# Performance work log

Measured on AMD Instinct MI355X. Metric: run time of the kernel, lower is better.

## Reference

```python
import jax, jax.numpy as jnp
import numpy as np

N = 131072   # total nodes
E = 262144   # directed edges (avg degree 2, molecular graphs)
G = 4096     # number of graphs in the batch
H = 64       # hidden_dim


def _linear_init(key, fan_in, fan_out):
    # torch.nn.Linear default: U(-1/sqrt(fan_in), 1/sqrt(fan_in))
    s = 1.0 / np.sqrt(fan_in)
    kw, kb = jax.random.split(key)
    W = jax.random.uniform(kw, (fan_in, fan_out), jnp.float32, -s, s)
    b = jax.random.uniform(kb, (fan_out,), jnp.float32, -s, s)
    return W, b


def setup_inputs() -> dict:
    key = jax.random.key(0)
    ks = jax.random.split(key, 8)
    d = {}
    d["x"] = jax.random.normal(ks[0], (N, 1), jnp.float32)
    d["edge_index"] = jax.random.randint(ks[1], (2, E), 0, N, jnp.int32)
    d["batch"] = jnp.sort(jax.random.randint(ks[2], (N,), 0, G, jnp.int32))
    d["W1"], d["b1"] = _linear_init(ks[3], 1, H)          # GCNConv(1, 64)
    d["W2"], d["b2"] = _linear_init(ks[4], H, 2 * H)       # GCNConv(64, 128)
    d["W3"], d["b3"] = _linear_init(ks[5], 2 * H, 4 * H)   # GCNConv(128, 256)
    d["fc1_W"], d["fc1_b"] = _linear_init(ks[6], 4 * H, 128)
    d["fc2_W"], d["fc2_b"] = _linear_init(ks[7], 128, 12)
    return d


def gcn_conv(x, W, b, src, dst):
    """PyG GCNConv: D^-1/2 (A + I) D^-1/2 (x W) + b, self-loops added."""
    h = x @ W                                                   # [N, out]
    deg = jax.ops.segment_sum(jnp.ones(E, jnp.float32), dst, num_segments=N) + 1.0
    dinv = jax.lax.rsqrt(deg)                                   # [N]
    coef = dinv[src] * dinv[dst]                                # [E]
    agg = jax.ops.segment_sum(h[src] * coef[:, None], dst, num_segments=N)
    agg = agg + h * (dinv * dinv)[:, None]                      # self-loop term: h_i / deg_i
    return agg + b


def reference(x, edge_index, batch, W1, b1, W2, b2, W3, b3, fc1_W, fc1_b, fc2_W, fc2_b):
    src, dst = edge_index[0], edge_index[1]
    h = jax.nn.relu(gcn_conv(x, W1, b1, src, dst))
    h = jax.nn.relu(gcn_conv(h, W2, b2, src, dst))
    h = gcn_conv(h, W3, b3, src, dst)                            # [N, 256]
    # global_mean_pool over batch ids
    sums = jax.ops.segment_sum(h, batch, num_segments=G)         # [G, 256]
    cnts = jax.ops.segment_sum(jnp.ones(N, jnp.float32), batch, num_segments=G)
    g = sums / jnp.maximum(cnts, 1.0)[:, None]
    g = jax.nn.relu(g @ fc1_W + fc1_b)
    return g @ fc2_W + fc2_b                                     # [G, 12]
```

## Files before the change

### kernel.cpp

```cpp
#include <hip/hip_runtime.h>
#include <hip/hip_fp16.h>

#define NN 131072
#define EE 262144
#define GG 4096

typedef _Float16 h2v __attribute__((ext_vector_type(2)));

#if __has_builtin(__builtin_amdgcn_fdot2)
#define FDOT2(a, b, c) __builtin_amdgcn_fdot2((a), (b), (c), false)
#else
#define FDOT2(a, b, c) ((float)(a)[0] * (float)(b)[0] + (float)(a)[1] * (float)(b)[1] + (c))
#endif

__global__ void k_zero(int4* __restrict__ p, int n4) {
    int i = blockIdx.x * 256 + threadIdx.x;
    if (i < n4) p[i] = make_int4(0, 0, 0, 0);
}

__global__ void k_count(const int* __restrict__ dst, int* __restrict__ indeg) {
    int e = blockIdx.x * 256 + threadIdx.x;
    if (e < EE) atomicAdd(&indeg[dst[e]], 1);
}

__global__ __launch_bounds__(256) void k_scan_a(const int* __restrict__ indeg,
                                                int* __restrict__ bsum,
                                                float* __restrict__ dinv,
                                                const int* __restrict__ batch,
                                                int* __restrict__ gstart) {
    __shared__ int red[256];
    int tid = threadIdx.x;
    int gid = blockIdx.x * 256 + tid;
    int v = indeg[gid];
    dinv[gid] = rsqrtf((float)v + 1.0f);
    red[tid] = v;
    {
        int b1v = batch[gid];
        int b0v = (gid == 0) ? -1 : batch[gid - 1];
        for (int g = b0v + 1; g <= b1v; ++g) gstart[g] = gid;
        if (gid == NN - 1)
            for (int g = b1v + 1; g <= GG; ++g) gstart[g] = NN;
    }
    __syncthreads();
#pragma unroll
    for (int off = 128; off > 0; off >>= 1) {
        if (tid < off) red[tid] += red[tid + off];
        __syncthreads();
    }
    if (tid == 0) bsum[blockIdx.x] = red[0];
}

__global__ __launch_bounds__(512) void k_scan_b(const int* __restrict__ bsum,
                                                int* __restrict__ boff) {
    __shared__ int ps[512];
    int tid = threadIdx.x;
    ps[tid] = bsum[tid];
    __syncthreads();
    for (int off = 1; off < 512; off <<= 1) {
        int v = (tid >= off) ? ps[tid - off] : 0;
        __syncthreads();
        ps[tid] += v;
        __syncthreads();
    }
    boff[tid] = (tid > 0) ? ps[tid - 1] : 0;
    if (tid == 511) boff[512] = ps[511];
}

__global__ __launch_bounds__(256) void k_scan_c(const int* __restrict__ indeg,
                                                const int* __restrict__ boff,
                                                int* __restrict__ rowptr,
                                                int* __restrict__ cursor) {
    __shared__ int ps[256];
    int tid = threadIdx.x;
    int gid = blockIdx.x * 256 + tid;
    int v = indeg[gid];
    ps[tid] = v;
    __syncthreads();
    for (int off = 1; off < 256; off <<= 1) {
        int t = (tid >= off) ? ps[tid - off] : 0;
        __syncthreads();
        ps[tid] += t;
        __syncthreads();
    }
    int excl = boff[blockIdx.x] + ps[tid] - v;
    rowptr[gid] = excl;
    cursor[gid] = excl;
    if (gid == NN - 1) rowptr[NN] = boff[512];
}

__global__ void k_fill_edges(const int* __restrict__ src, const int* __restrict__ dst,
                             const float* __restrict__ dinv,
                             int* __restrict__ cursor, int* __restrict__ ecol,
                             float* __restrict__ ecoef) {
    int e = blockIdx.x * 256 + threadIdx.x;
    if (e < EE) {
        int d = dst[e], s = src[e];
        int slot = atomicAdd(&cursor[d], 1);
        ecol[slot] = s;
        ecoef[slot] = dinv[d] * dinv[s];
    }
}

__global__ void k_z(const float* __restrict__ x, const float* __restrict__ dinv,
                    const int* __restrict__ rowptr, const int* __restrict__ ecol,
                    const float* __restrict__ ecoef, float* __restrict__ z) {
    int i = blockIdx.x * 256 + threadIdx.x;
    if (i < NN) {
        float di = dinv[i];
        float s = x[i] * di * di;
        int e0 = rowptr[i], e1 = rowptr[i + 1];
        for (int e = e0; e < e1; ++e) s += ecoef[e] * x[ecol[e]];
        z[i] = s;
    }
}

__global__ __launch_bounds__(256) void k_gemm2u(const float* __restrict__ z,
                                                const float* __restrict__ dinv,
                                                const int* __restrict__ rowptr,
                                                const int* __restrict__ ecol,
                                                const float* __restrict__ ecoef,
                                                const float* __restrict__ W1,
                                                const float* __restrict__ b1,
                                                const float* __restrict__ W2,
                                                const float* __restrict__ b2,
                                                __half* __restrict__ rh) {
    __shared__ h2v At[64][33];
    __shared__ h2v Wt[32][128];
    __shared__ float w1s[64], b1s[64];

    int tid = threadIdx.x;
    int i0 = blockIdx.x * 64;

    if (tid < 64) { w1s[tid] = W1[tid]; b1s[tid] = b1[tid]; }
    {
        int c4 = tid & 31, kp0 = tid >> 5;
#pragma unroll
        for (int p = 0; p < 4; ++p) {
            int kp = kp0 + p * 8;
            const float4 lo = *(const float4*)&W2[(size_t)(2 * kp) * 128 + c4 * 4];
            const float4 hi = *(const float4*)&W2[(size_t)(2 * kp + 1) * 128 + c4 * 4];
            h2v h0, h1, h2_, h3;
            h0[0] = (_Float16)lo.x; h0[1] = (_Float16)hi.x;
            h1[0] = (_Float16)lo.y; h1[1] = (_Float16)hi.y;
            h2_[0] = (_Float16)lo.z; h2_[1] = (_Float16)hi.z;
            h3[0] = (_Float16)lo.w; h3[1] = (_Float16)hi.w;
            Wt[kp][c4 * 4 + 0] = h0;
            Wt[kp][c4 * 4 + 1] = h1;
            Wt[kp][c4 * 4 + 2] = h2_;
            Wt[kp][c4 * 4 + 3] = h3;
        }
    }
    __syncthreads();

    {
        int n = tid >> 2;
        int kp0 = (tid & 3) * 8;
        int i = i0 + n;
        float zi = z[i], di = dinv[i];
        float d2 = di * di;
        float uacc[16];
#pragma unroll
        for (int j = 0; j < 16; ++j)
            uacc[j] = d2 * fmaxf(zi * w1s[kp0 * 2 + j] + b1s[kp0 * 2 + j], 0.f);
        int e0 = rowptr[i], e1 = rowptr[i + 1];
        for (int e = e0; e < e1; ++e) {
            float w = ecoef[e];
            float zs = z[ecol[e]];
#pragma unroll
            for (int j = 0; j < 16; ++j)
                uacc[j] += w * fmaxf(zs * w1s[kp0 * 2 + j] + b1s[kp0 * 2 + j], 0.f);
        }
#pragma unroll
        for (int j2 = 0; j2 < 8; ++j2) {
            h2v h;
            h[0] = (_Float16)uacc[2 * j2];
            h[1] = (_Float16)uacc[2 * j2 + 1];
            At[n][kp0 + j2] = h;
        }
    }
    __syncthreads();

    int colg = tid & 15;
    int rowg = tid >> 4;
    float acc[4][8];
#pragma unroll
    for (int rr = 0; rr < 4; ++rr)
#pragma unroll
        for (int c = 0; c < 8; ++c) acc[rr][c] = 0.0f;

#pragma unroll 4
    for (int kp = 0; kp < 32; ++kp) {
        h2v a2[4];
#pragma unroll
        for (int rr = 0; rr < 4; ++rr) a2[rr] = At[rowg * 4 + rr][kp];
        h2v wv[8];
        *(float4*)&wv[0] = *(const float4*)&Wt[kp][colg * 4];
        *(float4*)&wv[4] = *(const float4*)&Wt[kp][64 + colg * 4];
#pragma unroll
        for (int rr = 0; rr < 4; ++rr)
#pragma unroll
            for (int c = 0; c < 8; ++c)
                acc[rr][c] = FDOT2(a2[rr], wv[c], acc[rr][c]);
    }

#pragma unroll
    for (int rr = 0; rr < 4; ++rr) {
        int i = i0 + rowg * 4 + rr;
#pragma unroll
        for (int h = 0; h < 2; ++h) {
            int j = h * 64 + colg * 4;
            const float4 b = *(const float4*)&b2[j];
            __half2 p0 = __floats2half2_rn(fmaxf(acc[rr][h * 4 + 0] + b.x, 0.f),
                                           fmaxf(acc[rr][h * 4 + 1] + b.y, 0.f));
            __half2 p1 = __floats2half2_rn(fmaxf(acc[rr][h * 4 + 2] + b.z, 0.f),
                                           fmaxf(acc[rr][h * 4 + 3] + b.w, 0.f));
            union { __half2 h2[2]; float2 f; } u;
            u.h2[0] = p0; u.h2[1] = p1;
            *(float2*)&rh[(size_t)i * 128 + j] = u.f;
        }
    }
}

__device__ inline void ldr8(const __half* __restrict__ rh, size_t idx, float* o) {
    union { float4 f; __half2 h[4]; } u;
    u.f = *(const float4*)&rh[idx];
#pragma unroll
    for (int q = 0; q < 4; ++q) {
        float2 t = __half22float2(u.h[q]);
        o[q * 2] = t.x; o[q * 2 + 1] = t.y;
    }
}

__global__ __launch_bounds__(256) void k_pool(const __half* __restrict__ rh,
                                              const float* __restrict__ dinv,
                                              const int* __restrict__ rowptr,
                                              const int* __restrict__ ecol,
                                              const float* __restrict__ ecoef,
                                              const int* __restrict__ gstart,
                                              float* __restrict__ Y,
                                              float* __restrict__ cntf) {
    int g = blockIdx.x, tid = threadIdx.x;
    int lo = gstart[g], hi = gstart[g + 1];
    int cnt = hi - lo;

    int lane = tid & 15, ty = tid >> 4;
    int c = lane * 8;
    float acc[8];
#pragma unroll
    for (int q = 0; q < 8; ++q) acc[q] = 0.f;
    float v0[8], v1[8], v2[8], v3[8];

    int i = lo + ty;
    for (; i + 16 < hi; i += 32) {
        float d0 = dinv[i], d1 = dinv[i + 16];
        ldr8(rh, (size_t)i * 128 + c, v0);
        ldr8(rh, (size_t)(i + 16) * 128 + c, v1);
        float w0 = d0 * d0, w1 = d1 * d1;
#pragma unroll
        for (int q = 0; q < 8; ++q) acc[q] += v0[q] * w0 + v1[q] * w1;
    }
    for (; i < hi; i += 16) {
        float di = dinv[i], d2 = di * di;
        ldr8(rh, (size_t)i * 128 + c, v0);
#pragma unroll
        for (int q = 0; q < 8; ++q) acc[q] += v0[q] * d2;
    }

    int e0 = rowptr[lo], e1 = rowptr[hi];
    int e = e0 + ty;
    for (; e + 48 < e1; e += 64) {
        int s0 = ecol[e], s1 = ecol[e + 16], s2 = ecol[e + 32], s3 = ecol[e + 48];
        float w0 = ecoef[e], w1 = ecoef[e + 16], w2 = ecoef[e + 32], w3 = ecoef[e + 48];
        ldr8(rh, (size_t)s0 * 128 + c, v0);
        ldr8(rh, (size_t)s1 * 128 + c, v1);
        ldr8(rh, (size_t)s2 * 128 + c, v2);
        ldr8(rh, (size_t)s3 * 128 + c, v3);
#pragma unroll
        for (int q = 0; q < 8; ++q)
            acc[q] += v0[q] * w0 + v1[q] * w1 + v2[q] * w2 + v3[q] * w3;
    }
    for (; e < e1; e += 16) {
        int s = ecol[e];
        float w = ecoef[e];
        ldr8(rh, (size_t)s * 128 + c, v0);
#pragma unroll
        for (int q = 0; q < 8; ++q) acc[q] += v0[q] * w;
    }

    __shared__ float red[16][128];
    *(float4*)&red[ty][c]     = make_float4(acc[0], acc[1], acc[2], acc[3]);
    *(float4*)&red[ty][c + 4] = make_float4(acc[4], acc[5], acc[6], acc[7]);
    __syncthreads();
    if (tid < 128) {
        float s = 0.0f;
#pragma unroll
        for (int t = 0; t < 16; ++t) s += red[t][tid];
        float inv = (cnt > 0) ? 1.0f / (float)cnt : 0.0f;
        Y[(size_t)g * 128 + tid] = s * inv;
    }
    if (tid == 0) cntf[g] = (float)cnt;
}

template <int K, int OUTW, bool RELU_OUT, bool GUARD>
__global__ __launch_bounds__(256) void k_gemm(const float* __restrict__ A,
                                              const float* __restrict__ W,
                                              const float* __restrict__ bias,
                                              const float* __restrict__ cntf,
                                              float* __restrict__ C) {
    __shared__ float At[64][68];
    __shared__ float Wt[64][128];

    int tid  = threadIdx.x;
    int colg = tid & 15;
    int rowg = tid >> 4;
    int i0 = blockIdx.x * 64;
    int j0 = blockIdx.y * 128;

    float acc[4][8];
#pragma unroll
    for (int r = 0; r < 4; ++r)
#pragma unroll
        for (int c = 0; c < 8; ++c) acc[r][c] = 0.0f;

    for (int k0 = 0; k0 < K; k0 += 64) {
        __syncthreads();
        {
            int k4 = tid & 15, r0 = tid >> 4;
#pragma unroll
            for (int p = 0; p < 4; ++p) {
                int r = r0 + p * 16;
                *(float4*)&At[r][k4 * 4] =
                    *(const float4*)&A[(size_t)(i0 + r) * K + k0 + k4 * 4];
            }
        }
        {
            int c4 = tid & 31, kk0 = tid >> 5;
#pragma unroll
            for (int p = 0; p < 8; ++p) {
                int kk = kk0 + p * 8;
                *(float4*)&Wt[kk][c4 * 4] =
                    *(const float4*)&W[(size_t)(k0 + kk) * OUTW + j0 + c4 * 4];
            }
        }
        __syncthreads();
#pragma unroll 4
        for (int kk = 0; kk < 64; ++kk) {
            float a[4];
#pragma unroll
            for (int r = 0; r < 4; ++r) a[r] = At[rowg * 4 + r][kk];
            const float4 w0 = *(const float4*)&Wt[kk][colg * 4];
            const float4 w1 = *(const float4*)&Wt[kk][64 + colg * 4];
            float w[8] = {w0.x, w0.y, w0.z, w0.w, w1.x, w1.y, w1.z, w1.w};
#pragma unroll
            for (int r = 0; r < 4; ++r)
#pragma unroll
                for (int c = 0; c < 8; ++c) acc[r][c] += a[r] * w[c];
        }
    }

#pragma unroll
    for (int r = 0; r < 4; ++r) {
        int i = i0 + rowg * 4 + r;
        float flag = 1.0f;
        if (GUARD) flag = (cntf[i] > 0.0f) ? 1.0f : 0.0f;
#pragma unroll
        for (int h = 0; h < 2; ++h) {
            int j = j0 + h * 64 + colg * 4;
            const float4 b = *(const float4*)&bias[j];
            float4 v;
            v.x = acc[r][h * 4 + 0] + b.x * flag;
            v.y = acc[r][h * 4 + 1] + b.y * flag;
            v.z = acc[r][h * 4 + 2] + b.z * flag;
            v.w = acc[r][h * 4 + 3] + b.w * flag;
            if (RELU_OUT) {
                v.x = fmaxf(v.x, 0.f); v.y = fmaxf(v.y, 0.f);
                v.z = fmaxf(v.z, 0.f); v.w = fmaxf(v.w, 0.f);
            }
            *(float4*)&C[(size_t)i * OUTW + j] = v;
        }
    }
}

__global__ __launch_bounds__(256) void k_fc12(const float* __restrict__ A,
                                              const float* __restrict__ W,
                                              const float* __restrict__ bias,
                                              const float* __restrict__ fc2W,
                                              const float* __restrict__ fc2b,
                                              float* __restrict__ out) {
    __shared__ float At[64][68];
    __shared__ float Wt[64][128];

    int tid  = threadIdx.x;
    int colg = tid & 15;
    int rowg = tid >> 4;
    int i0 = blockIdx.x * 64;

    float acc[4][8];
#pragma unroll
    for (int r = 0; r < 4; ++r)
#pragma unroll
        for (int c = 0; c < 8; ++c) acc[r][c] = 0.0f;

    for (int k0 = 0; k0 < 256; k0 += 64) {
        __syncthreads();
        {
            int k4 = tid & 15, r0 = tid >> 4;
#pragma unroll
            for (int p = 0; p < 4; ++p) {
                int r = r0 + p * 16;
                *(float4*)&At[r][k4 * 4] =
                    *(const float4*)&A[(size_t)(i0 + r) * 256 + k0 + k4 * 4];
            }
        }
        {
            int c4 = tid & 31, kk0 = tid >> 5;
#pragma unroll
            for (int p = 0; p < 8; ++p) {
                int kk = kk0 + p * 8;
                *(float4*)&Wt[kk][c4 * 4] =
                    *(const float4*)&W[(size_t)(k0 + kk) * 128 + c4 * 4];
            }
        }
        __syncthreads();
#pragma unroll 4
        for (int kk = 0; kk < 64; ++kk) {
            float a[4];
#pragma unroll
            for (int r = 0; r < 4; ++r) a[r] = At[rowg * 4 + r][kk];
            const float4 w0 = *(const float4*)&Wt[kk][colg * 4];
            const float4 w1 = *(const float4*)&Wt[kk][64 + colg * 4];
            float w[8] = {w0.x, w0.y, w0.z, w0.w, w1.x, w1.y, w1.z, w1.w};
#pragma unroll
            for (int r = 0; r < 4; ++r)
#pragma unroll
                for (int c = 0; c < 8; ++c) acc[r][c] += a[r] * w[c];
        }
    }
    __syncthreads();
    float* g1s = &Wt[0][0];
    float* w2s = &At[0][0];
    for (int idx = tid; idx < 128 * 12; idx += 256) w2s[idx] = fc2W[idx];

#pragma unroll
    for (int r = 0; r < 4; ++r) {
        int row = rowg * 4 + r;
#pragma unroll
        for (int h = 0; h < 2; ++h) {
            int j = h * 64 + colg * 4;
            const float4 b = *(const float4*)&bias[j];
            float4 v;
            v.x = fmaxf(acc[r][h * 4 + 0] + b.x, 0.f);
            v.y = fmaxf(acc[r][h * 4 + 1] + b.y, 0.f);
            v.z = fmaxf(acc[r][h * 4 + 2] + b.z, 0.f);
            v.w = fmaxf(acc[r][h * 4 + 3] + b.w, 0.f);
            *(float4*)&g1s[row * 128 + j] = v;
        }
    }
    __syncthreads();
    for (int idx = tid; idx < 64 * 12; idx += 256) {
        int row = idx / 12, col = idx % 12;
        float o = fc2b[col];
        const float* gr = &g1s[row * 128];
        for (int k = 0; k < 128; ++k) o += gr[k] * w2s[k * 12 + col];
        out[(size_t)(i0 + row) * 12 + col] = o;
    }
}

extern "C" void kernel_launch(void* const* d_in, const int* in_sizes, int n_in,
                              void* d_out, int out_size, void* d_ws, size_t ws_size,
                              hipStream_t stream) {
    const float* x     = (const float*)d_in[0];
    const int*   ei    = (const int*)d_in[1];
    const int*   batch = (const int*)d_in[2];
    const float* W1    = (const float*)d_in[3];
    const float* b1    = (const float*)d_in[4];
    const float* W2    = (const float*)d_in[5];
    const float* b2    = (const float*)d_in[6];
    const float* W3    = (const float*)d_in[7];
    const float* b3    = (const float*)d_in[8];
    const float* fc1W  = (const float*)d_in[9];
    const float* fc1b  = (const float*)d_in[10];
    const float* fc2W  = (const float*)d_in[11];
    const float* fc2b  = (const float*)d_in[12];
    float* out = (float*)d_out;

    const int* srcp = ei;
    const int* dstp = ei + EE;

    float* ws     = (float*)d_ws;
    __half* rh    = (__half*)ws;
    float* Y      = ws + (size_t)NN * 64;
    float* pooled = Y + (size_t)GG * 128;
    float* cntf   = pooled + (size_t)GG * 256;
    float* dinv   = cntf + GG;
    float* zbuf   = dinv + NN;
    float* ecoef  = zbuf + NN;
    int* indeg  = (int*)(ecoef + EE);
    int* rowptr = indeg + NN;
    int* cursor = rowptr + NN + 4;
    int* ecol   = cursor + NN;
    int* bsum   = ecol + EE;
    int* boff   = bsum + 512;
    int* gstart = boff + 516;

    k_zero<<<NN / 4 / 256, 256, 0, stream>>>((int4*)indeg, NN / 4);
    k_count<<<EE / 256, 256, 0, stream>>>(dstp, indeg);
    k_scan_a<<<NN / 256, 256, 0, stream>>>(indeg, bsum, dinv, batch, gstart);
    k_scan_b<<<1, 512, 0, stream>>>(bsum, boff);
    k_scan_c<<<NN / 256, 256, 0, stream>>>(indeg, boff, rowptr, cursor);
    k_fill_edges<<<EE / 256, 256, 0, stream>>>(srcp, dstp, dinv, cursor, ecol, ecoef);

    k_z<<<NN / 256, 256, 0, stream>>>(x, dinv, rowptr, ecol, ecoef, zbuf);

    k_gemm2u<<<NN / 64, 256, 0, stream>>>(zbuf, dinv, rowptr, ecol, ecoef,
                                          W1, b1, W2, b2, rh);

    k_pool<<<GG, 256, 0, stream>>>(rh, dinv, rowptr, ecol, ecoef, gstart, Y, cntf);

    k_gemm<128, 256, false, true><<<dim3(GG / 64, 2), 256, 0, stream>>>(
        Y, W3, b3, cntf, pooled);
    k_fc12<<<GG / 64, 256, 0, stream>>>(pooled, fc1W, fc1b, fc2W, fc2b, out);
}
```

Baseline: 130.4 us.

## Fuse CSR build and first aggregation into one cooperative kernel with grid syncs

Replaces seven small kernel launches (zeroing, degree counting, three scan phases, edge fill, first-layer aggregation) with a single cooperative kernel of 512 blocks that separates the phases with grid-wide barriers. The aim is to remove per-launch overhead and inter-kernel gaps in the front-end. In exchange it depends on all 512 blocks being co-resident, and grid.sync may cost as much as the launches it replaces.

```diff
diff --git a/kernel.cpp b/kernel.cpp
--- a/kernel.cpp
+++ b/kernel.cpp
@@ -1,5 +1,8 @@
 #include <hip/hip_runtime.h>
 #include <hip/hip_fp16.h>
+#include <hip/hip_cooperative_groups.h>
+
+namespace cg = cooperative_groups;
 
 #define NN 131072
 #define EE 262144
@@ -13,99 +16,106 @@
 #define FDOT2(a, b, c) ((float)(a)[0] * (float)(b)[0] + (float)(a)[1] * (float)(b)[1] + (c))
 #endif
 
-__global__ void k_zero(int4* __restrict__ p, int n4) {
-    int i = blockIdx.x * 256 + threadIdx.x;
-    if (i < n4) p[i] = make_int4(0, 0, 0, 0);
-}
-
-__global__ void k_count(const int* __restrict__ dst, int* __restrict__ indeg) {
-    int e = blockIdx.x * 256 + threadIdx.x;
-    if (e < EE) atomicAdd(&indeg[dst[e]], 1);
-}
-
-__global__ __launch_bounds__(256) void k_scan_a(const int* __restrict__ indeg,
-                                                int* __restrict__ bsum,
-                                                float* __restrict__ dinv,
-                                                const int* __restrict__ batch,
-                                                int* __restrict__ gstart) {
-    __shared__ int red[256];
-    int tid = threadIdx.x;
-    int gid = blockIdx.x * 256 + tid;
-    int v = indeg[gid];
-    dinv[gid] = rsqrtf((float)v + 1.0f);
-    red[tid] = v;
-    {
+__global__ __launch_bounds__(256) void k_front(const int* __restrict__ src,
+                                               const int* __restrict__ dst,
+                                               const float* __restrict__ x,
+                                               const int* __restrict__ batch,
+                                               int* __restrict__ indeg,
+                                               int* __restrict__ bsum,
+                                               int* __restrict__ boff,
+                                               float* __restrict__ dinv,
+                                               int* __restrict__ gstart,
+                                               int* __restrict__ rowptr,
+                                               int* __restrict__ cursor,
+                                               int* __restrict__ ecol,
+                                               float* __restrict__ ecoef,
+                                               float* __restrict__ z) {
+    cg::grid_group grid = cg::this_grid();
+    int tid = threadIdx.x, b = blockIdx.x;
+    __shared__ int sh[256];
+
+    indeg[b * 256 + tid] = 0;
+    grid.sync();
+
+    {
+        int e = b * 512 + tid;
+        atomicAdd(&indeg[dst[e]], 1);
+        atomicAdd(&indeg[dst[e + 256]], 1);
+    }
+    grid.sync();
+
+    {
+        int gid = b * 256 + tid;
+        int v = indeg[gid];
+        dinv[gid] = rsqrtf((float)v + 1.0f);
         int b1v = batch[gid];
         int b0v = (gid == 0) ? -1 : batch[gid - 1];
         for (int g = b0v + 1; g <= b1v; ++g) gstart[g] = gid;
         if (gid == NN - 1)
             for (int g = b1v + 1; g <= GG; ++g) gstart[g] = NN;
-    }
-    __syncthreads();
-#pragma unroll
-    for (int off = 128; off > 0; off >>= 1) {
-        if (tid < off) red[tid] += red[tid + off];
-        __syncthreads();
-    }
-    if (tid == 0) bsum[blockIdx.x] = red[0];
-}
-
-__global__ __launch_bounds__(512) void k_scan_b(const int* __restrict__ bsum,
-                                                int* __restrict__ boff) {
-    __shared__ int ps[512];
-    int tid = threadIdx.x;
-    ps[tid] = bsum[tid];
-    __syncthreads();
-    for (int off = 1; off < 512; off <<= 1) {
-        int v = (tid >= off) ? ps[tid - off] : 0;
-        __syncthreads();
-        ps[tid] += v;
-        __syncthreads();
-    }
-    boff[tid] = (tid > 0) ? ps[tid - 1] : 0;
-    if (tid == 511) boff[512] = ps[511];
-}
-
-__global__ __launch_bounds__(256) void k_scan_c(const int* __restrict__ indeg,
-                                                const int* __restrict__ boff,
-                                                int* __restrict__ rowptr,
-                                                int* __restrict__ cursor) {
-    __shared__ int ps[256];
-    int tid = threadIdx.x;
-    int gid = blockIdx.x * 256 + tid;
-    int v = indeg[gid];
-    ps[tid] = v;
-    __syncthreads();
-    for (int off = 1; off < 256; off <<= 1) {
-        int t = (tid >= off) ? ps[tid - off] : 0;
-        __syncthreads();
-        ps[tid] += t;
-        __syncthreads();
-    }
-    int excl = boff[blockIdx.x] + ps[tid] - v;
-    rowptr[gid] = excl;
-    cursor[gid] = excl;
-    if (gid == NN - 1) rowptr[NN] = boff[512];
-}
-
-__global__ void k_fill_edges(const int* __restrict__ src, const int* __restrict__ dst,
-                             const float* __restrict__ dinv,
-                             int* __restrict__ cursor, int* __restrict__ ecol,
-                             float* __restrict__ ecoef) {
-    int e = blockIdx.x * 256 + threadIdx.x;
-    if (e < EE) {
-        int d = dst[e], s = src[e];
-        int slot = atomicAdd(&cursor[d], 1);
-        ecol[slot] = s;
-        ecoef[slot] = dinv[d] * dinv[s];
-    }
-}
-
-__global__ void k_z(const float* __restrict__ x, const float* __restrict__ dinv,
-                    const int* __restrict__ rowptr, const int* __restrict__ ecol,
-                    const float* __restrict__ ecoef, float* __restrict__ z) {
-    int i = blockIdx.x * 256 + threadIdx.x;
-    if (i < NN) {
+        sh[tid] = v;
+        __syncthreads();
+#pragma unroll
+        for (int off = 128; off > 0; off >>= 1) {
+            if (tid < off) sh[tid] += sh[tid + off];
+            __syncthreads();
+        }
+        if (tid == 0) bsum[b] = sh[0];
+        __syncthreads();
+    }
+    grid.sync();
+
+    if (b == 0) {
+        int a0 = bsum[2 * tid], a1 = bsum[2 * tid + 1];
+        int pair = a0 + a1;
+        sh[tid] = pair;
+        __syncthreads();
+        for (int off = 1; off < 256; off <<= 1) {
+            int v = (tid >= off) ? sh[tid - off] : 0;
+            __syncthreads();
+            sh[tid] += v;
+            __syncthreads();
+        }
+        int incl = sh[tid];
+        int excl = incl - pair;
+        boff[2 * tid] = excl;
+        boff[2 * tid + 1] = excl + a0;
+        if (tid == 255) boff[512] = incl;
+    }
+    grid.sync();
+
+    {
+        int gid = b * 256 + tid;
+        int v = indeg[gid];
+        sh[tid] = v;
+        __syncthreads();
+        for (int off = 1; off < 256; off <<= 1) {
+            int t2 = (tid >= off) ? sh[tid - off] : 0;
+            __syncthreads();
+            sh[tid] += t2;
+            __syncthreads();
+        }
+        int excl = boff[b] + sh[tid] - v;
+        rowptr[gid] = excl;
+        cursor[gid] = excl;
+        if (gid == NN - 1) rowptr[NN] = boff[512];
+    }
+    grid.sync();
+
+    {
+#pragma unroll
+        for (int q = 0; q < 2; ++q) {
+            int e = b * 512 + tid + q * 256;
+            int d = dst[e], s = src[e];
+            int slot = atomicAdd(&cursor[d], 1);
+            ecol[slot] = s;
+            ecoef[slot] = dinv[d] * dinv[s];
+        }
+    }
+    grid.sync();
+
+    {
+        int i = b * 256 + tid;
         float di = dinv[i];
         float s = x[i] * di * di;
         int e0 = rowptr[i], e1 = rowptr[i + 1];
@@ -503,14 +513,16 @@
     int* boff   = bsum + 512;
     int* gstart = boff + 516;
 
-    k_zero<<<NN / 4 / 256, 256, 0, stream>>>((int4*)indeg, NN / 4);
-    k_count<<<EE / 256, 256, 0, stream>>>(dstp, indeg);
-    k_scan_a<<<NN / 256, 256, 0, stream>>>(indeg, bsum, dinv, batch, gstart);
-    k_scan_b<<<1, 512, 0, stream>>>(bsum, boff);
-    k_scan_c<<<NN / 256, 256, 0, stream>>>(indeg, boff, rowptr, cursor);
-    k_fill_edges<<<EE / 256, 256, 0, stream>>>(srcp, dstp, dinv, cursor, ecol, ecoef);
-
-    k_z<<<NN / 256, 256, 0, stream>>>(x, dinv, rowptr, ecol, ecoef, zbuf);
+    {
+        void* args[] = {
+            (void*)&srcp, (void*)&dstp, (void*)&x, (void*)&batch,
+            (void*)&indeg, (void*)&bsum, (void*)&boff, (void*)&dinv,
+            (void*)&gstart, (void*)&rowptr, (void*)&cursor, (void*)&ecol,
+            (void*)&ecoef, (void*)&zbuf
+        };
+        hipLaunchCooperativeKernel((void*)k_front, dim3(512), dim3(256),
+                                   args, 0, stream);
+    }
 
     k_gemm2u<<<NN / 64, 256, 0, stream>>>(zbuf, dinv, rowptr, ecol, ecoef,
                                           W1, b1, W2, b2, rh);
```

Measured after the change: 451.0 us. 3.46x slower.
